# Kernel optimization log

Measured on AMD Instinct MI355X. Metric: run time of the kernel, lower is better.

The kernel has to match this reference:

```python
import jax, jax.numpy as jnp
import numpy as np

B, T, H = 256, 1024, 128

def _lstm_cell(x, h, c, W_ih, W_hh, b_ih, b_hh):
    # PyTorch LSTMCell gate order: i, f, g, o
    gates = x @ W_ih.T + b_ih + h @ W_hh.T + b_hh  # [B, 4H]
    i, f, g, o = jnp.split(gates, 4, axis=-1)
    c_new = jax.nn.sigmoid(f) * c + jax.nn.sigmoid(i) * jnp.tanh(g)
    h_new = jax.nn.sigmoid(o) * jnp.tanh(c_new)
    return h_new, c_new

def setup_inputs() -> dict:
    key = jax.random.key(0)
    ks = jax.random.split(key, 12)
    s = 1.0 / np.sqrt(H)
    u = lambda k, shape: jax.random.uniform(k, shape, jnp.float32, -s, s)
    return {
        "x": jax.random.normal(ks[0], (B, T, 1), jnp.float32),
        "W_ih1": u(ks[1], (4 * H, 1)),
        "W_hh1": u(ks[2], (4 * H, H)),
        "b_ih1": u(ks[3], (4 * H,)),
        "b_hh1": u(ks[4], (4 * H,)),
        "W_ih2": u(ks[5], (4 * H, H)),
        "W_hh2": u(ks[6], (4 * H, H)),
        "b_ih2": u(ks[7], (4 * H,)),
        "b_hh2": u(ks[8], (4 * H,)),
        "W_out": u(ks[9], (1, H)),
        "b_out": u(ks[10], (1,)),
    }

def reference(x, W_ih1, W_hh1, b_ih1, b_hh1, W_ih2, W_hh2, b_ih2, b_hh2, W_out, b_out):
    n = x.shape[0]
    z = jnp.zeros((n, H), jnp.float32)

    def step(carry, x_t):  # x_t: [B, 1]
        h1, c1, h2, c2 = carry
        h1, c1 = _lstm_cell(x_t, h1, c1, W_ih1, W_hh1, b_ih1, b_hh1)
        h2, c2 = _lstm_cell(h1, h2, c2, W_ih2, W_hh2, b_ih2, b_hh2)
        out = h2 @ W_out.T + b_out  # [B, 1]
        return (h1, c1, h2, c2), out

    xs = jnp.transpose(x, (1, 0, 2))  # [T, B, 1]
    _, outs = jax.lax.scan(step, (z, z, z, z), xs)  # outs: [T, B, 1]
    return jnp.transpose(outs[..., 0], (1, 0))  # [B, T]
```

## Files before the change

kernel.cpp:

```cpp
#include <hip/hip_runtime.h>
#include <hip/hip_fp16.h>
#include <stdint.h>

#define T_STEPS 1024
#define HDIM    128
#define NT      512


typedef _Float16 v2h __attribute__((ext_vector_type(2)));
union HU { uint32_t u; v2h v; };

#define SCL  1.44269504088896340736f
#define K2C  2.88538008177792681472f

__device__ __forceinline__ float dot2h(uint32_t a, uint32_t b, float c) {
    HU ua, ub; ua.u = a; ub.u = b;
    return __builtin_amdgcn_fdot2(ua.v, ub.v, c, false);
}
__device__ __forceinline__ uint32_t packh2s(float2 e) {
    return (uint32_t)__half_as_ushort(__float2half_rn(e.x * SCL)) |
           ((uint32_t)__half_as_ushort(__float2half_rn(e.y * SCL)) << 16);
}
__device__ __forceinline__ uint16_t f2h(float f) {
    return __half_as_ushort(__float2half_rn(f));
}
__device__ __forceinline__ float act2(float a2, float m) {
    return 1.0f - m * __builtin_amdgcn_rcpf(
        __builtin_amdgcn_exp2f(m * a2) + 1.0f);
}
__device__ __forceinline__ float tanhc(float c) {
    return 1.0f - 2.0f * __builtin_amdgcn_rcpf(
        __builtin_amdgcn_exp2f(K2C * c) + 1.0f);
}
__device__ __forceinline__ float red2(float v) {
    int iv = __float_as_int(v);
    v += __int_as_float(__builtin_amdgcn_update_dpp(0, iv, 0xB1, 0xF, 0xF, true));
    iv = __float_as_int(v);
    v += __int_as_float(__builtin_amdgcn_update_dpp(0, iv, 0x4E, 0xF, 0xF, true));
    return v;
}

#define SB() __builtin_amdgcn_sched_barrier(0)
#define PIN4(W) asm volatile("" : "+v"(W.x), "+v"(W.y), "+v"(W.z), "+v"(W.w))

#define SETW16(Wa, Wb, Wc, Wd, P) do { const float2* _r = (const float2*)(P); \
    Wa = make_uint4(packh2s(_r[0]),  packh2s(_r[1]),                       \
                    packh2s(_r[2]),  packh2s(_r[3]));                      \
    Wb = make_uint4(packh2s(_r[4]),  packh2s(_r[5]),                       \
                    packh2s(_r[6]),  packh2s(_r[7]));                      \
    Wc = make_uint4(packh2s(_r[8]),  packh2s(_r[9]),                       \
                    packh2s(_r[10]), packh2s(_r[11]));                     \
    Wd = make_uint4(packh2s(_r[12]), packh2s(_r[13]),                      \
                    packh2s(_r[14]), packh2s(_r[15])); } while (0)

#define ROW(Wa, Wb, Wc, Wd, P) do {                                        \
    SETW16(Wa, Wb, Wc, Wd, P);                                             \
    PIN4(Wa); PIN4(Wb); PIN4(Wc); PIN4(Wd); SB(); } while (0)

#define DOT8(Wa, Wb, H0, H1, acc) do {                                     \
    acc = dot2h(Wa.x, H0.x, acc); acc = dot2h(Wa.y, H0.y, acc);            \
    acc = dot2h(Wa.z, H0.z, acc); acc = dot2h(Wa.w, H0.w, acc);            \
    acc = dot2h(Wb.x, H1.x, acc); acc = dot2h(Wb.y, H1.y, acc);            \
    acc = dot2h(Wb.z, H1.z, acc); acc = dot2h(Wb.w, H1.w, acc); } while (0)

__global__ __launch_bounds__(NT)
__attribute__((amdgpu_waves_per_eu(2, 2)))
void lstm_persistent(
    const float* __restrict__ x,
    const float* __restrict__ W_ih1, const float* __restrict__ W_hh1,
    const float* __restrict__ b_ih1, const float* __restrict__ b_hh1,
    const float* __restrict__ W_ih2, const float* __restrict__ W_hh2,
    const float* __restrict__ b_ih2, const float* __restrict__ b_hh2,
    const float* __restrict__ W_out, const float* __restrict__ b_out,
    float* __restrict__ out)
{
    const int b   = blockIdx.x;
    const int tid = threadIdx.x;
    const int w   = tid >> 6;
    const int l   = tid & 63;
    const int s   = l & 3;
    const int e   = (w << 4) | (l >> 2);
    const int co  = s << 5;

    __shared__ __align__(16) uint32_t h1p[2][HDIM / 2];
    __shared__ __align__(16) uint32_t h2p[2][HDIM / 2];
    __shared__ float pbuf[2][8];

    uint4 m1_00,m1_01,m1_02,m1_03, m1_10,m1_11,m1_12,m1_13;
    uint4 m1_20,m1_21,m1_22,m1_23, m1_30,m1_31,m1_32,m1_33;
    uint4 m2_00,m2_01,m2_02,m2_03, m2_10,m2_11,m2_12,m2_13;
    uint4 m2_20,m2_21,m2_22,m2_23, m2_30,m2_31,m2_32,m2_33;
    uint4 m3_00,m3_01,m3_02,m3_03, m3_10,m3_11,m3_12,m3_13;
    uint4 m3_20,m3_21,m3_22,m3_23, m3_30,m3_31,m3_32,m3_33;
    {
        const float* p = W_hh1 + e * HDIM + co;
        ROW(m1_00,m1_01,m1_02,m1_03, p);
        ROW(m1_10,m1_11,m1_12,m1_13, p + 128 * HDIM);
        ROW(m1_20,m1_21,m1_22,m1_23, p + 256 * HDIM);
        ROW(m1_30,m1_31,m1_32,m1_33, p + 384 * HDIM);
        p = W_ih2 + e * HDIM + co;
        ROW(m2_00,m2_01,m2_02,m2_03, p);
        ROW(m2_10,m2_11,m2_12,m2_13, p + 128 * HDIM);
        ROW(m2_20,m2_21,m2_22,m2_23, p + 256 * HDIM);
        ROW(m2_30,m2_31,m2_32,m2_33, p + 384 * HDIM);
        p = W_hh2 + e * HDIM + co;
        ROW(m3_00,m3_01,m3_02,m3_03, p);
        ROW(m3_10,m3_11,m3_12,m3_13, p + 128 * HDIM);
        ROW(m3_20,m3_21,m3_22,m3_23, p + 256 * HDIM);
        ROW(m3_30,m3_31,m3_32,m3_33, p + 384 * HDIM);
    }

    const float b1i = (b_ih1[e]       + b_hh1[e])       * SCL;
    const float b1f = (b_ih1[e + 128] + b_hh1[e + 128]) * SCL;
    const float b1g = (b_ih1[e + 256] + b_hh1[e + 256]) * SCL;
    const float b1o = (b_ih1[e + 384] + b_hh1[e + 384]) * SCL;
    const float wxi = W_ih1[e]       * SCL, wxf = W_ih1[e + 128] * SCL;
    const float wxg = W_ih1[e + 256] * SCL, wxo = W_ih1[e + 384] * SCL;
    const float b2i = (b_ih2[e]       + b_hh2[e])       * SCL;
    const float b2f = (b_ih2[e + 128] + b_hh2[e + 128]) * SCL;
    const float b2g = (b_ih2[e + 256] + b_hh2[e + 256]) * SCL;
    const float b2o = (b_ih2[e + 384] + b_hh2[e + 384]) * SCL;
    const float wo = (s == 0) ? W_out[e] : 0.0f;
    const float bo = b_out[0];

    float c1 = 0.f, c2 = 0.f;

    if (tid < HDIM / 2) {
        h1p[0][tid] = 0u; h1p[1][tid] = 0u;
        h2p[0][tid] = 0u; h2p[1][tid] = 0u;
    }
    __syncthreads();

    const float* xb = x + b * T_STEPS;
    float*       ob = out + b * T_STEPS;
    float x_cur = xb[0];

    for (int k = 0; k <= T_STEPS; ++k) {
        const int rb = k & 1, wbuf = rb ^ 1;
        float x_nxt = xb[(k + 1 < T_STEPS) ? (k + 1) : (T_STEPS - 1)];

        const uint4* H1 = (const uint4*)h1p[rb];
        uint4 Ha0 = H1[4*s+0], Ha1 = H1[4*s+1];
        uint4 Hb0 = H1[4*s+2], Hb1 = H1[4*s+3];
        float a0=0.f,a1=0.f,a2=0.f,a3=0.f, q0=0.f,q1=0.f,q2=0.f,q3=0.f;
        DOT8(m1_00,m1_01, Ha0,Ha1, a0); DOT8(m1_10,m1_11, Ha0,Ha1, a1);
        DOT8(m1_20,m1_21, Ha0,Ha1, a2); DOT8(m1_30,m1_31, Ha0,Ha1, a3);
        DOT8(m1_02,m1_03, Hb0,Hb1, a0); DOT8(m1_12,m1_13, Hb0,Hb1, a1);
        DOT8(m1_22,m1_23, Hb0,Hb1, a2); DOT8(m1_32,m1_33, Hb0,Hb1, a3);
        DOT8(m2_00,m2_01, Ha0,Ha1, q0); DOT8(m2_10,m2_11, Ha0,Ha1, q1);
        DOT8(m2_20,m2_21, Ha0,Ha1, q2); DOT8(m2_30,m2_31, Ha0,Ha1, q3);
        DOT8(m2_02,m2_03, Hb0,Hb1, q0); DOT8(m2_12,m2_13, Hb0,Hb1, q1);
        DOT8(m2_22,m2_23, Hb0,Hb1, q2); DOT8(m2_32,m2_33, Hb0,Hb1, q3);

        const uint4* H2 = (const uint4*)h2p[rb];
        uint4 Hc0 = H2[4*s+0], Hc1 = H2[4*s+1];
        uint4 Hd0 = H2[4*s+2], Hd1 = H2[4*s+3];

        if (k >= 2 && tid < 8) {
            float ssum = pbuf[wbuf][tid];
            ssum += __shfl_xor(ssum, 1, 64);
            ssum += __shfl_xor(ssum, 2, 64);
            ssum += __shfl_xor(ssum, 4, 64);
            if (tid == 0) ob[k - 2] = ssum + bo;
        }

        a0 = red2(a0); a1 = red2(a1); a2 = red2(a2); a3 = red2(a3);
        float gi = act2(a0 + fmaf(x_cur, wxi, b1i), 1.0f);
        float gf = act2(a1 + fmaf(x_cur, wxf, b1f), 1.0f);
        float gg = act2(a2 + fmaf(x_cur, wxg, b1g), 2.0f);
        float go = act2(a3 + fmaf(x_cur, wxo, b1o), 1.0f);
        c1 = fmaf(gf, c1, gi * gg);
        float h1v = go * tanhc(c1);
        if (s == 0) ((uint16_t*)h1p[wbuf])[e] = f2h(h1v);

        DOT8(m3_00,m3_01, Hc0,Hc1, q0); DOT8(m3_10,m3_11, Hc0,Hc1, q1);
        DOT8(m3_20,m3_21, Hc0,Hc1, q2); DOT8(m3_30,m3_31, Hc0,Hc1, q3);
        DOT8(m3_02,m3_03, Hd0,Hd1, q0); DOT8(m3_12,m3_13, Hd0,Hd1, q1);
        DOT8(m3_22,m3_23, Hd0,Hd1, q2); DOT8(m3_32,m3_33, Hd0,Hd1, q3);

        if (k > 0) {
            q0 = red2(q0); q1 = red2(q1); q2 = red2(q2); q3 = red2(q3);
            float hi = act2(q0 + b2i, 1.0f);
            float hf = act2(q1 + b2f, 1.0f);
            float hg = act2(q2 + b2g, 2.0f);
            float ho = act2(q3 + b2o, 1.0f);
            c2 = fmaf(hf, c2, hi * hg);
            float h2v = ho * tanhc(c2);
            if (s == 0) ((uint16_t*)h2p[wbuf])[e] = f2h(h2v);
            float part = wo * h2v;
            part += __shfl_xor(part, 4,  64);
            part += __shfl_xor(part, 8,  64);
            part += __shfl_xor(part, 16, 64);
            part += __shfl_xor(part, 32, 64);
            if (l == 0) pbuf[rb][w] = part;
        }
        __syncthreads();
        x_cur = x_nxt;
    }

    if (tid < 8) {
        float ssum = pbuf[T_STEPS & 1][tid];
        ssum += __shfl_xor(ssum, 1, 64);
        ssum += __shfl_xor(ssum, 2, 64);
        ssum += __shfl_xor(ssum, 4, 64);
        if (tid == 0) ob[T_STEPS - 1] = ssum + bo;
    }
}

extern "C" void kernel_launch(void* const* d_in, const int* in_sizes, int n_in,
                              void* d_out, int out_size, void* d_ws, size_t ws_size,
                              hipStream_t stream) {
    const float* x     = (const float*)d_in[0];
    const float* W_ih1 = (const float*)d_in[1];
    const float* W_hh1 = (const float*)d_in[2];
    const float* b_ih1 = (const float*)d_in[3];
    const float* b_hh1 = (const float*)d_in[4];
    const float* W_ih2 = (const float*)d_in[5];
    const float* W_hh2 = (const float*)d_in[6];
    const float* b_ih2 = (const float*)d_in[7];
    const float* b_hh2 = (const float*)d_in[8];
    const float* W_out = (const float*)d_in[9];
    const float* b_out = (const float*)d_in[10];
    float* out = (float*)d_out;

    const int B = in_sizes[0] / T_STEPS;
    hipLaunchKernelGGL(lstm_persistent, dim3(B), dim3(NT), 0, stream,
                       x, W_ih1, W_hh1, b_ih1, b_hh1,
                       W_ih2, W_hh2, b_ih2, b_hh2, W_out, b_out, out);
}
```

Baseline: 1.538 ms.

## Process two batch rows per block sharing register-resident weights

Each block now runs two independent batch sequences, reusing the same packed fp16 weight registers for both and sharing one barrier per step. The grid shrinks to half the batch size. This is meant to amortize per-step sync and reduction latency and to add instruction-level parallelism from two independent dependency chains. In exchange it uses half as many blocks, more registers per thread and twice the math per step per block.

```diff
diff --git a/kernel.cpp b/kernel.cpp
--- a/kernel.cpp
+++ b/kernel.cpp
@@ -62,6 +62,9 @@
     acc = dot2h(Wa.z, H0.z, acc); acc = dot2h(Wa.w, H0.w, acc);            \
     acc = dot2h(Wb.x, H1.x, acc); acc = dot2h(Wb.y, H1.y, acc);            \
     acc = dot2h(Wb.z, H1.z, acc); acc = dot2h(Wb.w, H1.w, acc); } while (0)
+
+#define DOT8x2(Wa, Wb, HA0, HA1, accA, HB0, HB1, accB) do {                \
+    DOT8(Wa, Wb, HA0, HA1, accA); DOT8(Wa, Wb, HB0, HB1, accB); } while (0)
 
 __global__ __launch_bounds__(NT)
 __attribute__((amdgpu_waves_per_eu(2, 2)))
@@ -74,7 +77,7 @@
     const float* __restrict__ W_out, const float* __restrict__ b_out,
     float* __restrict__ out)
 {
-    const int b   = blockIdx.x;
+    const int b0  = blockIdx.x * 2;
     const int tid = threadIdx.x;
     const int w   = tid >> 6;
     const int l   = tid & 63;
@@ -82,9 +85,9 @@
     const int e   = (w << 4) | (l >> 2);
     const int co  = s << 5;
 
-    __shared__ __align__(16) uint32_t h1p[2][HDIM / 2];
-    __shared__ __align__(16) uint32_t h2p[2][HDIM / 2];
-    __shared__ float pbuf[2][8];
+    __shared__ __align__(16) uint32_t h1p[2][2][HDIM / 2];
+    __shared__ __align__(16) uint32_t h2p[2][2][HDIM / 2];
+    __shared__ float pbuf[2][2][8];
 
     uint4 m1_00,m1_01,m1_02,m1_03, m1_10,m1_11,m1_12,m1_13;
     uint4 m1_20,m1_21,m1_22,m1_23, m1_30,m1_31,m1_32,m1_33;
@@ -123,87 +126,151 @@
     const float wo = (s == 0) ? W_out[e] : 0.0f;
     const float bo = b_out[0];
 
-    float c1 = 0.f, c2 = 0.f;
+    float c1A = 0.f, c2A = 0.f, c1B = 0.f, c2B = 0.f;
 
     if (tid < HDIM / 2) {
-        h1p[0][tid] = 0u; h1p[1][tid] = 0u;
-        h2p[0][tid] = 0u; h2p[1][tid] = 0u;
+        h1p[0][0][tid] = 0u; h1p[1][0][tid] = 0u;
+        h1p[0][1][tid] = 0u; h1p[1][1][tid] = 0u;
+        h2p[0][0][tid] = 0u; h2p[1][0][tid] = 0u;
+        h2p[0][1][tid] = 0u; h2p[1][1][tid] = 0u;
     }
     __syncthreads();
 
-    const float* xb = x + b * T_STEPS;
-    float*       ob = out + b * T_STEPS;
-    float x_cur = xb[0];
+    const float* xbA = x + (size_t)b0 * T_STEPS;
+    const float* xbB = x + (size_t)(b0 + 1) * T_STEPS;
+    float* obA = out + (size_t)b0 * T_STEPS;
+    float* obB = out + (size_t)(b0 + 1) * T_STEPS;
+    float xcA = xbA[0], xcB = xbB[0];
 
     for (int k = 0; k <= T_STEPS; ++k) {
         const int rb = k & 1, wbuf = rb ^ 1;
-        float x_nxt = xb[(k + 1 < T_STEPS) ? (k + 1) : (T_STEPS - 1)];
-
-        const uint4* H1 = (const uint4*)h1p[rb];
-        uint4 Ha0 = H1[4*s+0], Ha1 = H1[4*s+1];
-        uint4 Hb0 = H1[4*s+2], Hb1 = H1[4*s+3];
-        float a0=0.f,a1=0.f,a2=0.f,a3=0.f, q0=0.f,q1=0.f,q2=0.f,q3=0.f;
-        DOT8(m1_00,m1_01, Ha0,Ha1, a0); DOT8(m1_10,m1_11, Ha0,Ha1, a1);
-        DOT8(m1_20,m1_21, Ha0,Ha1, a2); DOT8(m1_30,m1_31, Ha0,Ha1, a3);
-        DOT8(m1_02,m1_03, Hb0,Hb1, a0); DOT8(m1_12,m1_13, Hb0,Hb1, a1);
-        DOT8(m1_22,m1_23, Hb0,Hb1, a2); DOT8(m1_32,m1_33, Hb0,Hb1, a3);
-        DOT8(m2_00,m2_01, Ha0,Ha1, q0); DOT8(m2_10,m2_11, Ha0,Ha1, q1);
-        DOT8(m2_20,m2_21, Ha0,Ha1, q2); DOT8(m2_30,m2_31, Ha0,Ha1, q3);
-        DOT8(m2_02,m2_03, Hb0,Hb1, q0); DOT8(m2_12,m2_13, Hb0,Hb1, q1);
-        DOT8(m2_22,m2_23, Hb0,Hb1, q2); DOT8(m2_32,m2_33, Hb0,Hb1, q3);
-
-        const uint4* H2 = (const uint4*)h2p[rb];
-        uint4 Hc0 = H2[4*s+0], Hc1 = H2[4*s+1];
-        uint4 Hd0 = H2[4*s+2], Hd1 = H2[4*s+3];
-
-        if (k >= 2 && tid < 8) {
-            float ssum = pbuf[wbuf][tid];
-            ssum += __shfl_xor(ssum, 1, 64);
-            ssum += __shfl_xor(ssum, 2, 64);
-            ssum += __shfl_xor(ssum, 4, 64);
-            if (tid == 0) ob[k - 2] = ssum + bo;
-        }
-
-        a0 = red2(a0); a1 = red2(a1); a2 = red2(a2); a3 = red2(a3);
-        float gi = act2(a0 + fmaf(x_cur, wxi, b1i), 1.0f);
-        float gf = act2(a1 + fmaf(x_cur, wxf, b1f), 1.0f);
-        float gg = act2(a2 + fmaf(x_cur, wxg, b1g), 2.0f);
-        float go = act2(a3 + fmaf(x_cur, wxo, b1o), 1.0f);
-        c1 = fmaf(gf, c1, gi * gg);
-        float h1v = go * tanhc(c1);
-        if (s == 0) ((uint16_t*)h1p[wbuf])[e] = f2h(h1v);
-
-        DOT8(m3_00,m3_01, Hc0,Hc1, q0); DOT8(m3_10,m3_11, Hc0,Hc1, q1);
-        DOT8(m3_20,m3_21, Hc0,Hc1, q2); DOT8(m3_30,m3_31, Hc0,Hc1, q3);
-        DOT8(m3_02,m3_03, Hd0,Hd1, q0); DOT8(m3_12,m3_13, Hd0,Hd1, q1);
-        DOT8(m3_22,m3_23, Hd0,Hd1, q2); DOT8(m3_32,m3_33, Hd0,Hd1, q3);
+        int kn = (k + 1 < T_STEPS) ? (k + 1) : (T_STEPS - 1);
+        float xnA = xbA[kn], xnB = xbB[kn];
+
+        const uint4* HA = (const uint4*)h1p[rb][0];
+        const uint4* HB = (const uint4*)h1p[rb][1];
+        uint4 Aa0 = HA[4*s+0], Aa1 = HA[4*s+1], Ab0 = HA[4*s+2], Ab1 = HA[4*s+3];
+        uint4 Ba0 = HB[4*s+0], Ba1 = HB[4*s+1], Bb0 = HB[4*s+2], Bb1 = HB[4*s+3];
+        float aA0=0.f,aA1=0.f,aA2=0.f,aA3=0.f, qA0=0.f,qA1=0.f,qA2=0.f,qA3=0.f;
+        float aB0=0.f,aB1=0.f,aB2=0.f,aB3=0.f, qB0=0.f,qB1=0.f,qB2=0.f,qB3=0.f;
+        DOT8x2(m1_00,m1_01, Aa0,Aa1,aA0, Ba0,Ba1,aB0);
+        DOT8x2(m1_10,m1_11, Aa0,Aa1,aA1, Ba0,Ba1,aB1);
+        DOT8x2(m1_20,m1_21, Aa0,Aa1,aA2, Ba0,Ba1,aB2);
+        DOT8x2(m1_30,m1_31, Aa0,Aa1,aA3, Ba0,Ba1,aB3);
+        DOT8x2(m1_02,m1_03, Ab0,Ab1,aA0, Bb0,Bb1,aB0);
+        DOT8x2(m1_12,m1_13, Ab0,Ab1,aA1, Bb0,Bb1,aB1);
+        DOT8x2(m1_22,m1_23, Ab0,Ab1,aA2, Bb0,Bb1,aB2);
+        DOT8x2(m1_32,m1_33, Ab0,Ab1,aA3, Bb0,Bb1,aB3);
+        DOT8x2(m2_00,m2_01, Aa0,Aa1,qA0, Ba0,Ba1,qB0);
+        DOT8x2(m2_10,m2_11, Aa0,Aa1,qA1, Ba0,Ba1,qB1);
+        DOT8x2(m2_20,m2_21, Aa0,Aa1,qA2, Ba0,Ba1,qB2);
+        DOT8x2(m2_30,m2_31, Aa0,Aa1,qA3, Ba0,Ba1,qB3);
+        DOT8x2(m2_02,m2_03, Ab0,Ab1,qA0, Bb0,Bb1,qB0);
+        DOT8x2(m2_12,m2_13, Ab0,Ab1,qA1, Bb0,Bb1,qB1);
+        DOT8x2(m2_22,m2_23, Ab0,Ab1,qA2, Bb0,Bb1,qB2);
+        DOT8x2(m2_32,m2_33, Ab0,Ab1,qA3, Bb0,Bb1,qB3);
+
+        const uint4* GA = (const uint4*)h2p[rb][0];
+        const uint4* GB = (const uint4*)h2p[rb][1];
+        uint4 Ac0 = GA[4*s+0], Ac1 = GA[4*s+1], Ad0 = GA[4*s+2], Ad1 = GA[4*s+3];
+        uint4 Bc0 = GB[4*s+0], Bc1 = GB[4*s+1], Bd0 = GB[4*s+2], Bd1 = GB[4*s+3];
+
+        if (k >= 2) {
+            if (tid < 8) {
+                float ssum = pbuf[wbuf][0][tid];
+                ssum += __shfl_xor(ssum, 1, 64);
+                ssum += __shfl_xor(ssum, 2, 64);
+                ssum += __shfl_xor(ssum, 4, 64);
+                if (tid == 0) obA[k - 2] = ssum + bo;
+            } else if (tid >= 64 && tid < 72) {
+                float ssum = pbuf[wbuf][1][tid - 64];
+                ssum += __shfl_xor(ssum, 1, 64);
+                ssum += __shfl_xor(ssum, 2, 64);
+                ssum += __shfl_xor(ssum, 4, 64);
+                if (tid == 64) obB[k - 2] = ssum + bo;
+            }
+        }
+
+        aA0 = red2(aA0); aA1 = red2(aA1); aA2 = red2(aA2); aA3 = red2(aA3);
+        aB0 = red2(aB0); aB1 = red2(aB1); aB2 = red2(aB2); aB3 = red2(aB3);
+        {
+            float gi = act2(aA0 + fmaf(xcA, wxi, b1i), 1.0f);
+            float gf = act2(aA1 + fmaf(xcA, wxf, b1f), 1.0f);
+            float gg = act2(aA2 + fmaf(xcA, wxg, b1g), 2.0f);
+            float go = act2(aA3 + fmaf(xcA, wxo, b1o), 1.0f);
+            c1A = fmaf(gf, c1A, gi * gg);
+            float h1v = go * tanhc(c1A);
+            if (s == 0) ((uint16_t*)h1p[wbuf][0])[e] = f2h(h1v);
+        }
+        {
+            float gi = act2(aB0 + fmaf(xcB, wxi, b1i), 1.0f);
+            float gf = act2(aB1 + fmaf(xcB, wxf, b1f), 1.0f);
+            float gg = act2(aB2 + fmaf(xcB, wxg, b1g), 2.0f);
+            float go = act2(aB3 + fmaf(xcB, wxo, b1o), 1.0f);
+            c1B = fmaf(gf, c1B, gi * gg);
+            float h1v = go * tanhc(c1B);
+            if (s == 0) ((uint16_t*)h1p[wbuf][1])[e] = f2h(h1v);
+        }
+
+        DOT8x2(m3_00,m3_01, Ac0,Ac1,qA0, Bc0,Bc1,qB0);
+        DOT8x2(m3_10,m3_11, Ac0,Ac1,qA1, Bc0,Bc1,qB1);
+        DOT8x2(m3_20,m3_21, Ac0,Ac1,qA2, Bc0,Bc1,qB2);
+        DOT8x2(m3_30,m3_31, Ac0,Ac1,qA3, Bc0,Bc1,qB3);
+        DOT8x2(m3_02,m3_03, Ad0,Ad1,qA0, Bd0,Bd1,qB0);
+        DOT8x2(m3_12,m3_13, Ad0,Ad1,qA1, Bd0,Bd1,qB1);
+        DOT8x2(m3_22,m3_23, Ad0,Ad1,qA2, Bd0,Bd1,qB2);
+        DOT8x2(m3_32,m3_33, Ad0,Ad1,qA3, Bd0,Bd1,qB3);
 
         if (k > 0) {
-            q0 = red2(q0); q1 = red2(q1); q2 = red2(q2); q3 = red2(q3);
-            float hi = act2(q0 + b2i, 1.0f);
-            float hf = act2(q1 + b2f, 1.0f);
-            float hg = act2(q2 + b2g, 2.0f);
-            float ho = act2(q3 + b2o, 1.0f);
-            c2 = fmaf(hf, c2, hi * hg);
-            float h2v = ho * tanhc(c2);
-            if (s == 0) ((uint16_t*)h2p[wbuf])[e] = f2h(h2v);
-            float part = wo * h2v;
-            part += __shfl_xor(part, 4,  64);
-            part += __shfl_xor(part, 8,  64);
-            part += __shfl_xor(part, 16, 64);
-            part += __shfl_xor(part, 32, 64);
-            if (l == 0) pbuf[rb][w] = part;
+            qA0 = red2(qA0); qA1 = red2(qA1); qA2 = red2(qA2); qA3 = red2(qA3);
+            qB0 = red2(qB0); qB1 = red2(qB1); qB2 = red2(qB2); qB3 = red2(qB3);
+            float partA, partB;
+            {
+                float hi = act2(qA0 + b2i, 1.0f);
+                float hf = act2(qA1 + b2f, 1.0f);
+                float hg = act2(qA2 + b2g, 2.0f);
+                float ho = act2(qA3 + b2o, 1.0f);
+                c2A = fmaf(hf, c2A, hi * hg);
+                float h2v = ho * tanhc(c2A);
+                if (s == 0) ((uint16_t*)h2p[wbuf][0])[e] = f2h(h2v);
+                partA = wo * h2v;
+            }
+            {
+                float hi = act2(qB0 + b2i, 1.0f);
+                float hf = act2(qB1 + b2f, 1.0f);
+                float hg = act2(qB2 + b2g, 2.0f);
+                float ho = act2(qB3 + b2o, 1.0f);
+                c2B = fmaf(hf, c2B, hi * hg);
+                float h2v = ho * tanhc(c2B);
+                if (s == 0) ((uint16_t*)h2p[wbuf][1])[e] = f2h(h2v);
+                partB = wo * h2v;
+            }
+            partA += __shfl_xor(partA, 4,  64);
+            partA += __shfl_xor(partA, 8,  64);
+            partA += __shfl_xor(partA, 16, 64);
+            partA += __shfl_xor(partA, 32, 64);
+            partB += __shfl_xor(partB, 4,  64);
+            partB += __shfl_xor(partB, 8,  64);
+            partB += __shfl_xor(partB, 16, 64);
+            partB += __shfl_xor(partB, 32, 64);
+            if (l == 0) { pbuf[rb][0][w] = partA; pbuf[rb][1][w] = partB; }
         }
         __syncthreads();
-        x_cur = x_nxt;
+        xcA = xnA; xcB = xnB;
     }
 
     if (tid < 8) {
-        float ssum = pbuf[T_STEPS & 1][tid];
+        float ssum = pbuf[T_STEPS & 1][0][tid];
         ssum += __shfl_xor(ssum, 1, 64);
         ssum += __shfl_xor(ssum, 2, 64);
         ssum += __shfl_xor(ssum, 4, 64);
-        if (tid == 0) ob[T_STEPS - 1] = ssum + bo;
+        if (tid == 0) obA[T_STEPS - 1] = ssum + bo;
+    } else if (tid >= 64 && tid < 72) {
+        float ssum = pbuf[T_STEPS & 1][1][tid - 64];
+        ssum += __shfl_xor(ssum, 1, 64);
+        ssum += __shfl_xor(ssum, 2, 64);
+        ssum += __shfl_xor(ssum, 4, 64);
+        if (tid == 64) obB[T_STEPS - 1] = ssum + bo;
     }
 }
 
@@ -224,7 +291,7 @@
     float* out = (float*)d_out;
 
     const int B = in_sizes[0] / T_STEPS;
-    hipLaunchKernelGGL(lstm_persistent, dim3(B), dim3(NT), 0, stream,
+    hipLaunchKernelGGL(lstm_persistent, dim3(B / 2), dim3(NT), 0, stream,
                        x, W_ih1, W_hh1, b_ih1, b_hh1,
                        W_ih2, W_hh2, b_ih2, b_hh2, W_out, b_out, out);
 }
```

After: 3.174 ms. 2.06x slower.
